# Kernel optimization log

Measured on AMD Instinct MI355X. Metric: run time of the kernel, lower is better.

The kernel has to match this reference:

```python
import jax, jax.numpy as jnp
import numpy as np

HIDDEN = 64
SEQ_LEN = 128
BATCH = 64
T_MAX = 20.0
BW = 1.0


def setup_inputs() -> dict:
    key = jax.random.key(0)
    ks = jax.random.split(key, 8)
    s = 1.0 / np.sqrt(HIDDEN)
    return {
        "rand_uniform_pool": jax.random.uniform(ks[0], (BATCH, SEQ_LEN), jnp.float32, 1e-6, 1.0),
        "expert_time": jax.random.uniform(ks[1], (BATCH, SEQ_LEN), jnp.float32, 0.0, 1.0),
        "W_ih": jax.random.uniform(ks[2], (4 * HIDDEN, 1), jnp.float32, -s, s),
        "W_hh": jax.random.uniform(ks[3], (4 * HIDDEN, HIDDEN), jnp.float32, -s, s),
        "b_ih": jax.random.uniform(ks[4], (4 * HIDDEN,), jnp.float32, -s, s),
        "b_hh": jax.random.uniform(ks[5], (4 * HIDDEN,), jnp.float32, -s, s),
        "V_w": jax.random.uniform(ks[6], (1, HIDDEN), jnp.float32, -s, s),
        "V_b": jax.random.uniform(ks[7], (1,), jnp.float32, -s, s),
    }


def _generate_time(rand_uniform_pool, W_ih, W_hh, b_ih, b_hh, V_w, V_b):
    # sequential rollout over SEQ_LEN steps (data-dependent recurrence)
    u_seq = rand_uniform_pool.T[:, :, None]  # [S, B, 1]

    def step(carry, u):
        hx, cx, cum = carry
        sigma = jax.nn.elu(hx @ V_w.T + V_b) + 1.0            # [B, 1]
        cum = cum + (-jnp.log(u)) / sigma                      # exponential inter-event time
        gates = cum @ W_ih.T + b_ih + hx @ W_hh.T + b_hh       # [B, 4H]
        i, f, g, o = jnp.split(gates, 4, axis=1)               # torch LSTMCell gate order
        cx = jax.nn.sigmoid(f) * cx + jax.nn.sigmoid(i) * jnp.tanh(g)
        hx = jax.nn.sigmoid(o) * jnp.tanh(cx)
        return (hx, cx, cum), cum[:, 0]

    init = (jnp.zeros((BATCH, HIDDEN), jnp.float32),
            jnp.zeros((BATCH, HIDDEN), jnp.float32),
            jnp.zeros((BATCH, 1), jnp.float32))
    _, cums = jax.lax.scan(step, init, u_seq)                  # [S, B]
    return cums.T                                              # [B, S]


def _reward(expert_time, learner_time):
    N = BATCH * SEQ_LEN
    t_l = learner_time.reshape(N)
    t_e = expert_time.reshape(N)
    m_l = ((t_l < T_MAX) & (t_l > 0)).astype(jnp.float32)
    m_e = ((t_e < T_MAX) & (t_e > 0)).astype(jnp.float32)

    def ksum(a, b, ma, mb):
        # ma^T exp(-(a-b)^2/bw) mb without storing more than one NxN matrix at a time
        K = jnp.exp(-((b[:, None] - a[None, :]) ** 2) / BW)    # [N, N]
        return jnp.dot(mb, K @ ma)

    ee = ksum(t_e, t_e, m_e, m_e)
    ll = ksum(t_l, t_l, m_l, m_l)
    le = ksum(t_l, t_e, m_l, m_e)
    return (ee + ll - 2.0 * le).reshape(1, 1)


def reference(rand_uniform_pool, expert_time, W_ih, W_hh, b_ih, b_hh, V_w, V_b):
    learner_time = _generate_time(rand_uniform_pool, W_ih, W_hh, b_ih, b_hh, V_w, V_b)
    loss = _reward(expert_time, learner_time)
    return loss
```

## Files before the change

### kernel.cpp

```cpp
#include <hip/hip_runtime.h>
#include <math.h>

#define HIDDEN 64
#define SEQ 128
#define BATCH 64
#define NPTS (BATCH * SEQ)
#define TMAXV 20.0f
#define L2E 1.4426950408889634f
#define LN2 0.6931471805599453f

__device__ __forceinline__ float fexp2(float x) { return __builtin_amdgcn_exp2f(x); }
__device__ __forceinline__ float flog2(float x) { return __builtin_amdgcn_logf(x); }
__device__ __forceinline__ float frcp(float x)  { return __builtin_amdgcn_rcpf(x); }
__device__ __forceinline__ float fsigmoid(float x) { return frcp(1.0f + fexp2(-x * L2E)); }
__device__ __forceinline__ float ftanh(float x)    { return 1.0f - 2.0f * frcp(1.0f + fexp2(2.0f * x * L2E)); }

__device__ __forceinline__ float wave_sum(float v) {
    v += __shfl_xor(v, 1);
    v += __shfl_xor(v, 2);
    v += __shfl_xor(v, 4);
    v += __shfl_xor(v, 8);
    v += __shfl_xor(v, 16);
    v += __shfl_xor(v, 32);
    return v;
}

__global__ __launch_bounds__(256) void gen_and_ee(
    const float* __restrict__ upool,
    const float* __restrict__ texp,
    const float* __restrict__ Wih,
    const float* __restrict__ Whh,
    const float* __restrict__ bih,
    const float* __restrict__ bhh,
    const float* __restrict__ Vw,
    const float* __restrict__ Vb,
    float* __restrict__ tl,
    float* __restrict__ out)
{
    __shared__ __align__(16) float hx_s[64];
    __shared__ float act_s[256];
    __shared__ float lu_s[SEQ];
    __shared__ float cum_s;
    __shared__ float2 qbuf[2048];

    const int bid = blockIdx.x;
    const int tid = threadIdx.x;

    if (bid < BATCH) {
        const int h = tid & 63;

        float w[64];
        const float4* wrow = (const float4*)(Whh + tid * 64);
        #pragma unroll
        for (int k4 = 0; k4 < 16; ++k4) {
            float4 v = wrow[k4];
            w[4 * k4 + 0] = v.x; w[4 * k4 + 1] = v.y;
            w[4 * k4 + 2] = v.z; w[4 * k4 + 3] = v.w;
        }
        const float bias = bih[tid] + bhh[tid];
        const float wih  = Wih[tid];
        const float vw   = (tid < 64) ? Vw[tid] : 0.0f;
        const float vb   = Vb[0];

        if (tid < SEQ) lu_s[tid] = -flog2(upool[bid * SEQ + tid]) * LN2;
        if (tid < 64) hx_s[tid] = 0.0f;

        float cx = 0.0f, hx = 0.0f;
        __syncthreads();

        float x0 = vb;
        float sigma0 = (x0 > 0.0f) ? (x0 + 1.0f) : fexp2(x0 * L2E);
        float cum = lu_s[0] * frcp(sigma0);
        if (tid == 0) { cum_s = cum; tl[bid * SEQ + 0] = cum; }
        __syncthreads();

        for (int s = 0; s < SEQ - 1; ++s) {
            float dot = 0.0f;
            const float4* h4 = (const float4*)hx_s;
            #pragma unroll
            for (int k4 = 0; k4 < 16; ++k4) {
                float4 hv = h4[k4];
                dot = fmaf(w[4 * k4 + 0], hv.x, dot);
                dot = fmaf(w[4 * k4 + 1], hv.y, dot);
                dot = fmaf(w[4 * k4 + 2], hv.z, dot);
                dot = fmaf(w[4 * k4 + 3], hv.w, dot);
            }
            float g = dot + bias + cum_s * wih;
            float a = ((tid >> 6) == 2) ? ftanh(g) : fsigmoid(g);
            act_s[tid] = a;
            __syncthreads();

            if (tid < 64) {
                float ig = act_s[h];
                float fg = act_s[64 + h];
                float gg = act_s[128 + h];
                float og = act_s[192 + h];
                cx = fg * cx + ig * gg;
                hx = og * ftanh(cx);
                hx_s[h] = hx;
                float v = wave_sum(hx * vw);
                float xx = v + vb;
                float sig = (xx > 0.0f) ? (xx + 1.0f) : fexp2(xx * L2E);
                cum += lu_s[s + 1] * frcp(sig);
                if (tid == 0) { cum_s = cum; tl[bid * SEQ + s + 1] = cum; }
            }
            __syncthreads();
        }
    } else {
        const int eb = bid - BATCH;
        const int pc = eb & 31;
        const int qs = eb >> 5;

        const int p = pc * 256 + tid;
        const float tp = texp[p];
        const float mp = (tp < TMAXV && tp > 0.0f) ? 1.0f : 0.0f;

        const int q0 = qs * 2048;
        for (int i = tid; i < 2048; i += 256) {
            float tq = texp[q0 + i];
            float mq = (tq < TMAXV && tq > 0.0f) ? 1.0f : 0.0f;
            qbuf[i] = make_float2(tq, mq);
        }
        __syncthreads();

        float acc = 0.0f;
        #pragma unroll 4
        for (int i = 0; i < 2048; ++i) {
            float2 qq = qbuf[i];
            float d = tp - qq.x;
            acc = fmaf(qq.y, fexp2(d * d * (-L2E)), acc);
        }
        acc *= mp;
        acc = wave_sum(acc);
        if ((tid & 63) == 0) atomicAdd(out, acc);
    }
}

__global__ __launch_bounds__(256) void ll_le(
    const float* __restrict__ texp,
    const float* __restrict__ tl,
    float* __restrict__ out)
{
    __shared__ __align__(16) float4 qbuf[512];
    __shared__ float red[4];

    const int pc = blockIdx.x;
    const int qs = blockIdx.y;
    const int tid = threadIdx.x;

    const int p = pc * 256 + tid;
    const float tlp = tl[p];
    const float mlp = (tlp < TMAXV && tlp > 0.0f) ? 1.0f : 0.0f;

    const int q0 = qs * 512;
    for (int i = tid; i < 512; i += 256) {
        float tq = tl[q0 + i];
        float mq = (tq < TMAXV && tq > 0.0f) ? 1.0f : 0.0f;
        float te = texp[q0 + i];
        float me = (te < TMAXV && te > 0.0f) ? 1.0f : 0.0f;
        qbuf[i] = make_float4(tq, mq, te, me);
    }
    __syncthreads();

    float a_ll = 0.0f, a_le = 0.0f;
    #pragma unroll 4
    for (int i = 0; i < 512; ++i) {
        float4 q = qbuf[i];
        float d1 = tlp - q.x;
        a_ll = fmaf(q.y, fexp2(d1 * d1 * (-L2E)), a_ll);
        float d2 = tlp - q.z;
        a_le = fmaf(q.w, fexp2(d2 * d2 * (-L2E)), a_le);
    }
    float val = mlp * (a_ll - 2.0f * a_le);

    val = wave_sum(val);
    if ((tid & 63) == 0) red[tid >> 6] = val;
    __syncthreads();
    if (tid == 0) atomicAdd(out, red[0] + red[1] + red[2] + red[3]);
}

extern "C" void kernel_launch(void* const* d_in, const int* in_sizes, int n_in,
                              void* d_out, int out_size, void* d_ws, size_t ws_size,
                              hipStream_t stream) {
    const float* upool = (const float*)d_in[0];
    const float* texp  = (const float*)d_in[1];
    const float* Wih   = (const float*)d_in[2];
    const float* Whh   = (const float*)d_in[3];
    const float* bih   = (const float*)d_in[4];
    const float* bhh   = (const float*)d_in[5];
    const float* Vw    = (const float*)d_in[6];
    const float* Vb    = (const float*)d_in[7];
    float* out = (float*)d_out;
    float* tl  = (float*)d_ws;

    hipMemsetAsync(out, 0, sizeof(float), stream);
    hipLaunchKernelGGL(gen_and_ee, dim3(BATCH + 128), dim3(256), 0, stream,
                       upool, texp, Wih, Whh, bih, bhh, Vw, Vb, tl, out);
    hipLaunchKernelGGL(ll_le, dim3(32, 16), dim3(256), 0, stream, texp, tl, out);
}
```

Before: 188.4 us.

## Replicate LSTM cell update per wave to drop a barrier per recurrence step

Every wave now computes the LSTM cell/hidden update redundantly and writes its own private copy of hx, with double-buffered activation storage. This removes the second __syncthreads per step and the shared cum broadcast. The cum reduction now uses DPP row operations plus readlane instead of shuffles, and the matvec uses packed two-wide float math. The ll_le kernel also skips the pairwise loop for waves whose learner points are all masked out. The cost is redundant transcendental work in all four waves and four times the hx shared storage.

Result: faster. 160.9 us (-14.6%).

```diff
diff --git a/kernel.cpp b/kernel.cpp
--- a/kernel.cpp
+++ b/kernel.cpp
@@ -9,19 +9,32 @@
 #define L2E 1.4426950408889634f
 #define LN2 0.6931471805599453f
 
+typedef float v2f __attribute__((ext_vector_type(2)));
+
 __device__ __forceinline__ float fexp2(float x) { return __builtin_amdgcn_exp2f(x); }
 __device__ __forceinline__ float flog2(float x) { return __builtin_amdgcn_logf(x); }
 __device__ __forceinline__ float frcp(float x)  { return __builtin_amdgcn_rcpf(x); }
 __device__ __forceinline__ float fsigmoid(float x) { return frcp(1.0f + fexp2(-x * L2E)); }
 __device__ __forceinline__ float ftanh(float x)    { return 1.0f - 2.0f * frcp(1.0f + fexp2(2.0f * x * L2E)); }
 
-__device__ __forceinline__ float wave_sum(float v) {
-    v += __shfl_xor(v, 1);
-    v += __shfl_xor(v, 2);
-    v += __shfl_xor(v, 4);
-    v += __shfl_xor(v, 8);
-    v += __shfl_xor(v, 16);
-    v += __shfl_xor(v, 32);
+template <int CTRL>
+__device__ __forceinline__ float dpp_mov(float x) {
+    int r = __builtin_amdgcn_update_dpp(0, __float_as_int(x), CTRL, 0xf, 0xf, false);
+    return __int_as_float(r);
+}
+__device__ __forceinline__ float wave_sum_dpp(float x) {
+    x += dpp_mov<0x111>(x);
+    x += dpp_mov<0x112>(x);
+    x += dpp_mov<0x114>(x);
+    x += dpp_mov<0x118>(x);
+    x += dpp_mov<0x142>(x);
+    x += dpp_mov<0x143>(x);
+    return __int_as_float(__builtin_amdgcn_readlane(__float_as_int(x), 63));
+}
+
+__device__ __forceinline__ float wave_sum_shfl(float v) {
+    v += __shfl_xor(v, 1);  v += __shfl_xor(v, 2);  v += __shfl_xor(v, 4);
+    v += __shfl_xor(v, 8);  v += __shfl_xor(v, 16); v += __shfl_xor(v, 32);
     return v;
 }
 
@@ -37,74 +50,71 @@
     float* __restrict__ tl,
     float* __restrict__ out)
 {
-    __shared__ __align__(16) float hx_s[64];
-    __shared__ float act_s[256];
     __shared__ float lu_s[SEQ];
-    __shared__ float cum_s;
+    __shared__ float act_s[2][256];
+    __shared__ __align__(16) float hx_s[4][64];
     __shared__ float2 qbuf[2048];
 
     const int bid = blockIdx.x;
     const int tid = threadIdx.x;
 
     if (bid < BATCH) {
-        const int h = tid & 63;
-
-        float w[64];
+        const int h  = tid & 63;
+        const int wv = tid >> 6;
+
+        v2f w2[32];
         const float4* wrow = (const float4*)(Whh + tid * 64);
         #pragma unroll
-        for (int k4 = 0; k4 < 16; ++k4) {
-            float4 v = wrow[k4];
-            w[4 * k4 + 0] = v.x; w[4 * k4 + 1] = v.y;
-            w[4 * k4 + 2] = v.z; w[4 * k4 + 3] = v.w;
+        for (int k = 0; k < 16; ++k) {
+            float4 v = wrow[k];
+            w2[2 * k]     = (v2f){v.x, v.y};
+            w2[2 * k + 1] = (v2f){v.z, v.w};
         }
         const float bias = bih[tid] + bhh[tid];
         const float wih  = Wih[tid];
-        const float vw   = (tid < 64) ? Vw[tid] : 0.0f;
+        const float vw   = Vw[h];
         const float vb   = Vb[0];
 
         if (tid < SEQ) lu_s[tid] = -flog2(upool[bid * SEQ + tid]) * LN2;
-        if (tid < 64) hx_s[tid] = 0.0f;
-
-        float cx = 0.0f, hx = 0.0f;
+        hx_s[wv][h] = 0.0f;
+        float cx = 0.0f;
         __syncthreads();
 
-        float x0 = vb;
-        float sigma0 = (x0 > 0.0f) ? (x0 + 1.0f) : fexp2(x0 * L2E);
-        float cum = lu_s[0] * frcp(sigma0);
-        if (tid == 0) { cum_s = cum; tl[bid * SEQ + 0] = cum; }
-        __syncthreads();
+        float sg0 = (vb > 0.0f) ? (vb + 1.0f) : fexp2(vb * L2E);
+        float cum = lu_s[0] * frcp(sg0);
+        if (tid == 0) tl[bid * SEQ + 0] = cum;
 
         for (int s = 0; s < SEQ - 1; ++s) {
-            float dot = 0.0f;
-            const float4* h4 = (const float4*)hx_s;
+            const float4* h4 = (const float4*)hx_s[wv];
+            v2f a0 = {0.f, 0.f}, a1 = {0.f, 0.f}, a2 = {0.f, 0.f}, a3 = {0.f, 0.f};
             #pragma unroll
-            for (int k4 = 0; k4 < 16; ++k4) {
-                float4 hv = h4[k4];
-                dot = fmaf(w[4 * k4 + 0], hv.x, dot);
-                dot = fmaf(w[4 * k4 + 1], hv.y, dot);
-                dot = fmaf(w[4 * k4 + 2], hv.z, dot);
-                dot = fmaf(w[4 * k4 + 3], hv.w, dot);
+            for (int k = 0; k < 16; k += 2) {
+                float4 va = h4[k];
+                float4 vbq = h4[k + 1];
+                a0 = a0 + w2[2 * k]     * (v2f){va.x, va.y};
+                a1 = a1 + w2[2 * k + 1] * (v2f){va.z, va.w};
+                a2 = a2 + w2[2 * k + 2] * (v2f){vbq.x, vbq.y};
+                a3 = a3 + w2[2 * k + 3] * (v2f){vbq.z, vbq.w};
             }
-            float g = dot + bias + cum_s * wih;
-            float a = ((tid >> 6) == 2) ? ftanh(g) : fsigmoid(g);
-            act_s[tid] = a;
+            v2f aa = (a0 + a1) + (a2 + a3);
+            float g = (aa.x + aa.y) + bias + cum * wih;
+            float a = (wv == 2) ? ftanh(g) : fsigmoid(g);
+            act_s[s & 1][tid] = a;
             __syncthreads();
 
-            if (tid < 64) {
-                float ig = act_s[h];
-                float fg = act_s[64 + h];
-                float gg = act_s[128 + h];
-                float og = act_s[192 + h];
-                cx = fg * cx + ig * gg;
-                hx = og * ftanh(cx);
-                hx_s[h] = hx;
-                float v = wave_sum(hx * vw);
-                float xx = v + vb;
-                float sig = (xx > 0.0f) ? (xx + 1.0f) : fexp2(xx * L2E);
-                cum += lu_s[s + 1] * frcp(sig);
-                if (tid == 0) { cum_s = cum; tl[bid * SEQ + s + 1] = cum; }
-            }
-            __syncthreads();
+            float ig = act_s[s & 1][h];
+            float fg = act_s[s & 1][64 + h];
+            float gg = act_s[s & 1][128 + h];
+            float og = act_s[s & 1][192 + h];
+            cx = fg * cx + ig * gg;
+            float hx = og * ftanh(cx);
+            hx_s[wv][h] = hx;
+
+            float tot = wave_sum_dpp(hx * vw);
+            float xx  = tot + vb;
+            float sg  = (xx > 0.0f) ? (xx + 1.0f) : fexp2(xx * L2E);
+            cum += lu_s[s + 1] * frcp(sg);
+            if (tid == 0) tl[bid * SEQ + s + 1] = cum;
         }
     } else {
         const int eb = bid - BATCH;
@@ -131,7 +141,7 @@
             acc = fmaf(qq.y, fexp2(d * d * (-L2E)), acc);
         }
         acc *= mp;
-        acc = wave_sum(acc);
+        acc = wave_sum_shfl(acc);
         if ((tid & 63) == 0) atomicAdd(out, acc);
     }
 }
@@ -162,18 +172,21 @@
     }
     __syncthreads();
 
-    float a_ll = 0.0f, a_le = 0.0f;
-    #pragma unroll 4
-    for (int i = 0; i < 512; ++i) {
-        float4 q = qbuf[i];
-        float d1 = tlp - q.x;
-        a_ll = fmaf(q.y, fexp2(d1 * d1 * (-L2E)), a_ll);
-        float d2 = tlp - q.z;
-        a_le = fmaf(q.w, fexp2(d2 * d2 * (-L2E)), a_le);
+    float val = 0.0f;
+    if (__ballot(mlp != 0.0f) != 0ULL) {
+        float a_ll = 0.0f, a_le = 0.0f;
+        #pragma unroll 4
+        for (int i = 0; i < 512; ++i) {
+            float4 q = qbuf[i];
+            float d1 = tlp - q.x;
+            a_ll = fmaf(q.y, fexp2(d1 * d1 * (-L2E)), a_ll);
+            float d2 = tlp - q.z;
+            a_le = fmaf(q.w, fexp2(d2 * d2 * (-L2E)), a_le);
+        }
+        val = mlp * (a_ll - 2.0f * a_le);
     }
-    float val = mlp * (a_ll - 2.0f * a_le);
-
-    val = wave_sum(val);
+
+    val = wave_sum_shfl(val);
     if ((tid & 63) == 0) red[tid >> 6] = val;
     __syncthreads();
     if (tid == 0) atomicAdd(out, red[0] + red[1] + red[2] + red[3]);
```
